# Performance work log

Hardware: AMD Instinct MI355X
Metric: run time of the kernel (lower is better)

## Reference

```python
import jax, jax.numpy as jnp
import numpy as np

D_MODEL = 1024
NHEAD = 16
HEAD_DIM = D_MODEL // NHEAD
SCALE = HEAD_DIM ** (-0.5)


def setup_inputs() -> dict:
    key = jax.random.key(0)
    k1, k2, k3 = jax.random.split(key, 3)
    B, T, C = 2, 2048, D_MODEL
    x = jax.random.normal(k1, (B, T, C), dtype=jnp.float32)
    W_qkv = jax.random.normal(k2, (3 * C, C), dtype=jnp.float32) * (C ** -0.5)
    b_qkv = jnp.zeros((3 * C,), dtype=jnp.float32)
    W_out = jax.random.normal(k3, (C, C), dtype=jnp.float32) * (C ** -0.5)
    b_out = jnp.zeros((C,), dtype=jnp.float32)
    return {"x": x, "W_qkv": W_qkv, "b_qkv": b_qkv, "W_out": W_out, "b_out": b_out}


def reference(x, W_qkv, b_qkv, W_out, b_out):
    B, T, C = x.shape
    H, hd = NHEAD, HEAD_DIM
    qkv = x @ W_qkv.T + b_qkv
    qkv = qkv.reshape(B, T, 3, H, hd).transpose(2, 0, 3, 1, 4)
    q, k, v = qkv[0], qkv[1], qkv[2]
    # scaled dot-product scores: (B,H,T,T)
    attn = jnp.einsum('bhqd,bhkd->bhqk', q, k) * SCALE
    # causal mask (is_causal=True): lower-triangular allowed
    causal = jnp.tril(jnp.ones((T, T), dtype=bool))
    attn = jnp.where(causal[None, None, :, :], attn, -jnp.inf)
    attn = jax.nn.softmax(attn, axis=-1)
    # (B,H,T,hd) -> (B,T,C)
    out = jnp.einsum('bhqk,bhkd->bhqd', attn, v)
    out = out.transpose(0, 2, 1, 3).reshape(B, T, C)
    out = out @ W_out.T + b_out
    return out
```

## Files before the change

### kernel.cpp

```cpp
#include <hip/hip_runtime.h>
#include <hip/hip_bf16.h>
#include <stdint.h>

#define D_MODEL 1024
#define NHEAD   16
#define HEAD_DIM 64
#define BATCH   2
#define SEQ     2048
#define M_TOK   (BATCH*SEQ)
#define N_QKV   (3*D_MODEL)
#define KDIM    1024
#define Q_SCALE (0.125f * 1.44269504088896f)

typedef __bf16 bf16_t;
typedef bf16_t bf16x8 __attribute__((ext_vector_type(8)));
typedef bf16_t bf16x4 __attribute__((ext_vector_type(4)));
typedef float  f32x4  __attribute__((ext_vector_type(4)));

__device__ __forceinline__ void gl_lds16(const void* g, void* l) {
    __builtin_amdgcn_global_load_lds(
        (__attribute__((address_space(1))) void*)(void*)(const_cast<void*>(g)),
        (__attribute__((address_space(3))) void*)l, 16, 0, 0);
}

#define N4_X  (M_TOK * KDIM / 4)
#define N4_W1 (N_QKV * KDIM / 4)
#define N4_W2 (D_MODEL * KDIM / 4)
__global__ void convert_all(const float* __restrict__ x,
                            const float* __restrict__ w1,
                            const float* __restrict__ w2,
                            bf16_t* __restrict__ ox,
                            bf16_t* __restrict__ o1,
                            bf16_t* __restrict__ o2) {
    int t = blockIdx.x * blockDim.x + threadIdx.x;
    const float* src;
    bf16_t* dst;
    int off;
    if (t < N4_X)                { src = x;  dst = ox; off = t; }
    else if (t < N4_X + N4_W1)   { src = w1; dst = o1; off = t - N4_X; }
    else                         { src = w2; dst = o2; off = t - N4_X - N4_W1; }
    float4 v = reinterpret_cast<const float4*>(src)[off];
    bf16x4 o = { (bf16_t)v.x, (bf16_t)v.y, (bf16_t)v.z, (bf16_t)v.w };
    reinterpret_cast<bf16x4*>(dst)[off] = o;
}

template <int MODE>
__global__ __launch_bounds__(256) void gemm_bt(
    const bf16_t* __restrict__ A,
    const bf16_t* __restrict__ Bw,
    const float*  __restrict__ bias,
    int N,
    bf16_t* __restrict__ qkv_out,
    bf16_t* __restrict__ vt_out,
    float*  __restrict__ f32_out)
{
    __shared__ bf16_t As[128 * 32];
    __shared__ bf16_t Bs[128 * 32];

    const int cpx = gridDim.x >> 3;
    const int bid = (blockIdx.x & 7) * cpx + (blockIdx.x >> 3);

    const int nbn = N / 128;
    const int bm = bid / nbn;
    const int bn = bid % nbn;
    const int m0 = bm * 128, n0 = bn * 128;
    const int tid = threadIdx.x, wave = tid >> 6, lane = tid & 63;
    const int wr = wave >> 1, wc = wave & 1;

    f32x4 acc[4][4] = {};

    const int srow = lane >> 2;
    const int scol = ((lane & 3) ^ ((lane >> 3) & 3)) * 8;
    const bf16_t* gA0 = A  + (size_t)(m0 + wave * 16 + srow) * KDIM + scol;
    const bf16_t* gB0 = Bw + (size_t)(n0 + wave * 16 + srow) * KDIM + scol;
    bf16_t* lA0 = &As[(wave * 16) * 32];
    bf16_t* lB0 = &Bs[(wave * 16) * 32];

    const int fr = lane & 15;
    const int ch = ((lane >> 4) ^ ((fr >> 1) & 3)) * 8;

    for (int k0 = 0; k0 < KDIM; k0 += 32) {
        gl_lds16(gA0 + k0,             lA0);
        gl_lds16(gA0 + 64 * KDIM + k0, lA0 + 64 * 32);
        gl_lds16(gB0 + k0,             lB0);
        gl_lds16(gB0 + 64 * KDIM + k0, lB0 + 64 * 32);
        __syncthreads();

        bf16x8 af[4], bfr[4];
#pragma unroll
        for (int i = 0; i < 4; i++)
            af[i] = *reinterpret_cast<const bf16x8*>(
                &As[(wr * 64 + i * 16 + fr) * 32 + ch]);
#pragma unroll
        for (int j = 0; j < 4; j++)
            bfr[j] = *reinterpret_cast<const bf16x8*>(
                &Bs[(wc * 64 + j * 16 + fr) * 32 + ch]);
#pragma unroll
        for (int i = 0; i < 4; i++)
#pragma unroll
            for (int j = 0; j < 4; j++)
                acc[i][j] = __builtin_amdgcn_mfma_f32_16x16x32_bf16(
                    af[i], bfr[j], acc[i][j], 0, 0, 0);
        __syncthreads();
    }

#pragma unroll
    for (int i = 0; i < 4; i++) {
#pragma unroll
        for (int j = 0; j < 4; j++) {
            const int col = n0 + wc * 64 + j * 16 + fr;
            const float bv = bias[col];
#pragma unroll
            for (int r = 0; r < 4; r++) {
                const int row = m0 + wr * 64 + i * 16 + (lane >> 4) * 4 + r;
                float v = acc[i][j][r] + bv;
                if (MODE == 0) {
                    const int s = col >> 10;
                    if (s == 0) {
                        qkv_out[(size_t)row * N_QKV + col] = (bf16_t)(v * Q_SCALE);
                    } else if (s == 1) {
                        qkv_out[(size_t)row * N_QKV + col] = (bf16_t)v;
                    } else {
                        const int rem = col & 1023;
                        const int h = rem >> 6, d = rem & 63;
                        const int b = row >> 11, t = row & 2047;
                        vt_out[((size_t)((b * NHEAD + h) * HEAD_DIM + d)) * SEQ + t] =
                            (bf16_t)v;
                    }
                } else {
                    f32_out[(size_t)row * N + col] = v;
                }
            }
        }
    }
}

__global__ __launch_bounds__(256) void attn_fwd(
    const bf16_t* __restrict__ qkv,
    const bf16_t* __restrict__ Vt,
    bf16_t* __restrict__ O)
{
    __shared__ bf16_t Ks[64 * 64];
    __shared__ bf16_t Vs[64 * 64];
    __shared__ bf16_t Ps[4][16 * 72];

    const int nqt = SEQ / 64;
    const int nbh = BATCH * NHEAD;
    const int qt = (nqt - 1) - (blockIdx.x / nbh);
    const int bh = blockIdx.x % nbh;
    const int b = bh >> 4, h = bh & 15;
    const int q0 = qt * 64;
    const int tid = threadIdx.x, wave = tid >> 6, lane = tid & 63;
    const int fr = lane & 15;
    const int kq = lane >> 4;
    const int sw = fr & 7;
    const int c0 = (kq ^ sw) * 8;
    const int c1 = ((kq + 4) ^ sw) * 8;

    bf16x8 qf[2];
    {
        const size_t qrow = (size_t)(b * SEQ + q0 + wave * 16 + fr);
        const int cbase = h * 64 + kq * 8;
        qf[0] = *reinterpret_cast<const bf16x8*>(&qkv[qrow * N_QKV + cbase]);
        qf[1] = *reinterpret_cast<const bf16x8*>(&qkv[qrow * N_QKV + cbase + 32]);
    }

    f32x4 acc_o[4] = {};
    float l_part = 0.f;

    const int srow = lane >> 3;
    const int scol = ((lane & 7) ^ srow) * 8;
    const bf16_t* gK = qkv + (size_t)(b * SEQ) * N_QKV + (D_MODEL + h * 64);
    const bf16_t* gV = Vt + (size_t)(bh * 64) * SEQ;

    const int ntiles = qt + 1;
    for (int it = 0; it < ntiles; ++it) {
        const int kv0 = it * 64;
#pragma unroll
        for (int c = 0; c < 2; c++) {
            const int row = c * 32 + wave * 8 + srow;
            gl_lds16(gK + (size_t)(kv0 + row) * N_QKV + scol,
                     &Ks[(c * 32 + wave * 8) * 64]);
            gl_lds16(gV + (size_t)row * SEQ + kv0 + scol,
                     &Vs[(c * 32 + wave * 8) * 64]);
        }
        __syncthreads();

        f32x4 s[4];
        __builtin_amdgcn_s_setprio(1);
#pragma unroll
        for (int j = 0; j < 4; j++) {
            bf16x8 k0f = *reinterpret_cast<const bf16x8*>(
                &Ks[(j * 16 + fr) * 64 + c0]);
            bf16x8 k1f = *reinterpret_cast<const bf16x8*>(
                &Ks[(j * 16 + fr) * 64 + c1]);
            f32x4 t = {0.f, 0.f, 0.f, 0.f};
            t = __builtin_amdgcn_mfma_f32_16x16x32_bf16(k0f, qf[0], t, 0, 0, 0);
            t = __builtin_amdgcn_mfma_f32_16x16x32_bf16(k1f, qf[1], t, 0, 0, 0);
            s[j] = t;
        }
        __builtin_amdgcn_s_setprio(0);

        if (it == ntiles - 1) {
            const int qg = wave * 16 + fr;
#pragma unroll
            for (int j = 0; j < 4; j++)
#pragma unroll
                for (int r = 0; r < 4; r++)
                    if (j * 16 + kq * 4 + r > qg) s[j][r] = -1e30f;
        }

        float rs = 0.f;
#pragma unroll
        for (int j = 0; j < 4; j++)
#pragma unroll
            for (int r = 0; r < 4; r++) {
                const float p = exp2f(s[j][r]);
                s[j][r] = p;
                rs += p;
            }
        l_part += rs;

#pragma unroll
        for (int j = 0; j < 4; j++) {
            bf16x4 pq = { (bf16_t)s[j][0], (bf16_t)s[j][1],
                          (bf16_t)s[j][2], (bf16_t)s[j][3] };
            *reinterpret_cast<bf16x4*>(&Ps[wave][fr * 72 + j * 16 + kq * 4]) = pq;
        }
        bf16x8 pb0 = *reinterpret_cast<const bf16x8*>(
            &Ps[wave][fr * 72 + kq * 8]);
        bf16x8 pb1 = *reinterpret_cast<const bf16x8*>(
            &Ps[wave][fr * 72 + 32 + kq * 8]);

        __builtin_amdgcn_s_setprio(1);
#pragma unroll
        for (int j = 0; j < 4; j++) {
            bf16x8 v0f = *reinterpret_cast<const bf16x8*>(
                &Vs[(j * 16 + fr) * 64 + c0]);
            bf16x8 v1f = *reinterpret_cast<const bf16x8*>(
                &Vs[(j * 16 + fr) * 64 + c1]);
            acc_o[j] = __builtin_amdgcn_mfma_f32_16x16x32_bf16(v0f, pb0, acc_o[j], 0, 0, 0);
            acc_o[j] = __builtin_amdgcn_mfma_f32_16x16x32_bf16(v1f, pb1, acc_o[j], 0, 0, 0);
        }
        __builtin_amdgcn_s_setprio(0);

        __syncthreads();
    }

    float l_run = l_part;
    l_run += __shfl_xor(l_run, 16);
    l_run += __shfl_xor(l_run, 32);
    const float inv = 1.0f / l_run;
    const size_t rowq = (size_t)(b * SEQ + q0 + wave * 16 + fr);
#pragma unroll
    for (int j = 0; j < 4; j++) {
        bf16x4 ov = { (bf16_t)(acc_o[j][0] * inv), (bf16_t)(acc_o[j][1] * inv),
                      (bf16_t)(acc_o[j][2] * inv), (bf16_t)(acc_o[j][3] * inv) };
        *reinterpret_cast<bf16x4*>(&O[rowq * D_MODEL + h * 64 + j * 16 + kq * 4]) = ov;
    }
}

extern "C" void kernel_launch(void* const* d_in, const int* in_sizes, int n_in,
                              void* d_out, int out_size, void* d_ws, size_t ws_size,
                              hipStream_t stream) {
    (void)in_sizes; (void)n_in; (void)out_size; (void)ws_size;
    const float* x    = (const float*)d_in[0];
    const float* Wqkv = (const float*)d_in[1];
    const float* bqkv = (const float*)d_in[2];
    const float* Wout = (const float*)d_in[3];
    const float* bout = (const float*)d_in[4];
    float* out = (float*)d_out;

    char* ws = (char*)d_ws;
    size_t off = 0;
    bf16_t* x_bf    = (bf16_t*)(ws + off); off += (size_t)M_TOK * KDIM * 2;
    bf16_t* wqkv_bf = (bf16_t*)(ws + off); off += (size_t)N_QKV * KDIM * 2;
    bf16_t* wout_bf = (bf16_t*)(ws + off); off += (size_t)D_MODEL * KDIM * 2;
    bf16_t* qkv     = (bf16_t*)(ws + off); off += (size_t)M_TOK * N_QKV * 2;
    bf16_t* vt      = (bf16_t*)(ws + off); off += (size_t)BATCH * NHEAD * HEAD_DIM * SEQ * 2;
    bf16_t* o_bf    = (bf16_t*)(ws + off); off += (size_t)M_TOK * D_MODEL * 2;

    convert_all<<<(N4_X + N4_W1 + N4_W2) / 256, 256, 0, stream>>>(
        x, Wqkv, Wout, x_bf, wqkv_bf, wout_bf);

    gemm_bt<0><<<(M_TOK / 128) * (N_QKV / 128), 256, 0, stream>>>(
        x_bf, wqkv_bf, bqkv, N_QKV, qkv, vt, nullptr);

    attn_fwd<<<BATCH * NHEAD * (SEQ / 64), 256, 0, stream>>>(qkv, vt, o_bf);

    gemm_bt<1><<<(M_TOK / 128) * (D_MODEL / 128), 256, 0, stream>>>(
        o_bf, wout_bf, bout, D_MODEL, nullptr, nullptr, out);
}
```

Baseline: 118.2 us.

## Process 32 query rows per wave in attention to reuse K/V fragments

```diff
diff --git a/kernel.cpp b/kernel.cpp
--- a/kernel.cpp
+++ b/kernel.cpp
@@ -135,14 +135,14 @@
     }
 }
 
-__global__ __launch_bounds__(256) void attn_fwd(
+__global__ __launch_bounds__(128) void attn_fwd(
     const bf16_t* __restrict__ qkv,
     const bf16_t* __restrict__ Vt,
     bf16_t* __restrict__ O)
 {
     __shared__ bf16_t Ks[64 * 64];
     __shared__ bf16_t Vs[64 * 64];
-    __shared__ bf16_t Ps[4][16 * 72];
+    __shared__ bf16_t Ps[2][32 * 72];
 
     const int nqt = SEQ / 64;
     const int nbh = BATCH * NHEAD;
@@ -157,16 +157,19 @@
     const int c0 = (kq ^ sw) * 8;
     const int c1 = ((kq + 4) ^ sw) * 8;
 
-    bf16x8 qf[2];
+    bf16x8 qf0[2], qf1[2];
     {
-        const size_t qrow = (size_t)(b * SEQ + q0 + wave * 16 + fr);
         const int cbase = h * 64 + kq * 8;
-        qf[0] = *reinterpret_cast<const bf16x8*>(&qkv[qrow * N_QKV + cbase]);
-        qf[1] = *reinterpret_cast<const bf16x8*>(&qkv[qrow * N_QKV + cbase + 32]);
-    }
-
-    f32x4 acc_o[4] = {};
-    float l_part = 0.f;
+        const size_t r0 = (size_t)(b * SEQ + q0 + wave * 32 + fr);
+        const size_t r1 = r0 + 16;
+        qf0[0] = *reinterpret_cast<const bf16x8*>(&qkv[r0 * N_QKV + cbase]);
+        qf0[1] = *reinterpret_cast<const bf16x8*>(&qkv[r0 * N_QKV + cbase + 32]);
+        qf1[0] = *reinterpret_cast<const bf16x8*>(&qkv[r1 * N_QKV + cbase]);
+        qf1[1] = *reinterpret_cast<const bf16x8*>(&qkv[r1 * N_QKV + cbase + 32]);
+    }
+
+    f32x4 acc0[4] = {}, acc1[4] = {};
+    float l0 = 0.f, l1 = 0.f;
 
     const int srow = lane >> 3;
     const int scol = ((lane & 7) ^ srow) * 8;
@@ -177,60 +180,84 @@
     for (int it = 0; it < ntiles; ++it) {
         const int kv0 = it * 64;
 #pragma unroll
-        for (int c = 0; c < 2; c++) {
-            const int row = c * 32 + wave * 8 + srow;
+        for (int c = 0; c < 4; c++) {
+            const int row = wave * 32 + c * 8 + srow;
             gl_lds16(gK + (size_t)(kv0 + row) * N_QKV + scol,
-                     &Ks[(c * 32 + wave * 8) * 64]);
+                     &Ks[(wave * 32 + c * 8) * 64]);
             gl_lds16(gV + (size_t)row * SEQ + kv0 + scol,
-                     &Vs[(c * 32 + wave * 8) * 64]);
+                     &Vs[(wave * 32 + c * 8) * 64]);
         }
         __syncthreads();
 
-        f32x4 s[4];
+        bf16x8 kf0[4], kf1[4];
+#pragma unroll
+        for (int j = 0; j < 4; j++) {
+            kf0[j] = *reinterpret_cast<const bf16x8*>(
+                &Ks[(j * 16 + fr) * 64 + c0]);
+            kf1[j] = *reinterpret_cast<const bf16x8*>(
+                &Ks[(j * 16 + fr) * 64 + c1]);
+        }
+
+        f32x4 s0[4], s1[4];
         __builtin_amdgcn_s_setprio(1);
 #pragma unroll
         for (int j = 0; j < 4; j++) {
-            bf16x8 k0f = *reinterpret_cast<const bf16x8*>(
-                &Ks[(j * 16 + fr) * 64 + c0]);
-            bf16x8 k1f = *reinterpret_cast<const bf16x8*>(
-                &Ks[(j * 16 + fr) * 64 + c1]);
             f32x4 t = {0.f, 0.f, 0.f, 0.f};
-            t = __builtin_amdgcn_mfma_f32_16x16x32_bf16(k0f, qf[0], t, 0, 0, 0);
-            t = __builtin_amdgcn_mfma_f32_16x16x32_bf16(k1f, qf[1], t, 0, 0, 0);
-            s[j] = t;
+            t = __builtin_amdgcn_mfma_f32_16x16x32_bf16(kf0[j], qf0[0], t, 0, 0, 0);
+            t = __builtin_amdgcn_mfma_f32_16x16x32_bf16(kf1[j], qf0[1], t, 0, 0, 0);
+            s0[j] = t;
+            f32x4 u = {0.f, 0.f, 0.f, 0.f};
+            u = __builtin_amdgcn_mfma_f32_16x16x32_bf16(kf0[j], qf1[0], u, 0, 0, 0);
+            u = __builtin_amdgcn_mfma_f32_16x16x32_bf16(kf1[j], qf1[1], u, 0, 0, 0);
+            s1[j] = u;
         }
         __builtin_amdgcn_s_setprio(0);
 
         if (it == ntiles - 1) {
-            const int qg = wave * 16 + fr;
+            const int qg0 = wave * 32 + fr;
+            const int qg1 = qg0 + 16;
 #pragma unroll
             for (int j = 0; j < 4; j++)
 #pragma unroll
-                for (int r = 0; r < 4; r++)
-                    if (j * 16 + kq * 4 + r > qg) s[j][r] = -1e30f;
-        }
-
-        float rs = 0.f;
+                for (int r = 0; r < 4; r++) {
+                    const int kvl = j * 16 + kq * 4 + r;
+                    if (kvl > qg0) s0[j][r] = -1e30f;
+                    if (kvl > qg1) s1[j][r] = -1e30f;
+                }
+        }
+
+        float rs0 = 0.f, rs1 = 0.f;
 #pragma unroll
         for (int j = 0; j < 4; j++)
 #pragma unroll
             for (int r = 0; r < 4; r++) {
-                const float p = exp2f(s[j][r]);
-                s[j][r] = p;
-                rs += p;
+                const float p0 = exp2f(s0[j][r]);
+                const float p1 = exp2f(s1[j][r]);
+                s0[j][r] = p0;
+                s1[j][r] = p1;
+                rs0 += p0;
+                rs1 += p1;
             }
-        l_part += rs;
-
-#pragma unroll
-        for (int j = 0; j < 4; j++) {
-            bf16x4 pq = { (bf16_t)s[j][0], (bf16_t)s[j][1],
-                          (bf16_t)s[j][2], (bf16_t)s[j][3] };
-            *reinterpret_cast<bf16x4*>(&Ps[wave][fr * 72 + j * 16 + kq * 4]) = pq;
-        }
+        l0 += rs0;
+        l1 += rs1;
+
+#pragma unroll
+        for (int j = 0; j < 4; j++) {
+            bf16x4 p0 = { (bf16_t)s0[j][0], (bf16_t)s0[j][1],
+                          (bf16_t)s0[j][2], (bf16_t)s0[j][3] };
+            *reinterpret_cast<bf16x4*>(&Ps[wave][fr * 72 + j * 16 + kq * 4]) = p0;
+            bf16x4 p1 = { (bf16_t)s1[j][0], (bf16_t)s1[j][1],
+                          (bf16_t)s1[j][2], (bf16_t)s1[j][3] };
+            *reinterpret_cast<bf16x4*>(&Ps[wave][(16 + fr) * 72 + j * 16 + kq * 4]) = p1;
+        }
+        bf16x8 pa0 = *reinterpret_cast<const bf16x8*>(
+            &Ps[wave][fr * 72 + kq * 8]);
+        bf16x8 pa1 = *reinterpret_cast<const bf16x8*>(
+            &Ps[wave][fr * 72 + 32 + kq * 8]);
         bf16x8 pb0 = *reinterpret_cast<const bf16x8*>(
-            &Ps[wave][fr * 72 + kq * 8]);
+            &Ps[wave][(16 + fr) * 72 + kq * 8]);
         bf16x8 pb1 = *reinterpret_cast<const bf16x8*>(
-            &Ps[wave][fr * 72 + 32 + kq * 8]);
+            &Ps[wave][(16 + fr) * 72 + 32 + kq * 8]);
 
         __builtin_amdgcn_s_setprio(1);
 #pragma unroll
@@ -239,24 +266,32 @@
                 &Vs[(j * 16 + fr) * 64 + c0]);
             bf16x8 v1f = *reinterpret_cast<const bf16x8*>(
                 &Vs[(j * 16 + fr) * 64 + c1]);
-            acc_o[j] = __builtin_amdgcn_mfma_f32_16x16x32_bf16(v0f, pb0, acc_o[j], 0, 0, 0);
-            acc_o[j] = __builtin_amdgcn_mfma_f32_16x16x32_bf16(v1f, pb1, acc_o[j], 0, 0, 0);
+            acc0[j] = __builtin_amdgcn_mfma_f32_16x16x32_bf16(v0f, pa0, acc0[j], 0, 0, 0);
+            acc0[j] = __builtin_amdgcn_mfma_f32_16x16x32_bf16(v1f, pa1, acc0[j], 0, 0, 0);
+            acc1[j] = __builtin_amdgcn_mfma_f32_16x16x32_bf16(v0f, pb0, acc1[j], 0, 0, 0);
+            acc1[j] = __builtin_amdgcn_mfma_f32_16x16x32_bf16(v1f, pb1, acc1[j], 0, 0, 0);
         }
         __builtin_amdgcn_s_setprio(0);
 
         __syncthreads();
     }
 
-    float l_run = l_part;
-    l_run += __shfl_xor(l_run, 16);
-    l_run += __shfl_xor(l_run, 32);
-    const float inv = 1.0f / l_run;
-    const size_t rowq = (size_t)(b * SEQ + q0 + wave * 16 + fr);
+    l0 += __shfl_xor(l0, 16);
+    l0 += __shfl_xor(l0, 32);
+    l1 += __shfl_xor(l1, 16);
+    l1 += __shfl_xor(l1, 32);
+    const float inv0 = 1.0f / l0;
+    const float inv1 = 1.0f / l1;
+    const size_t row0 = (size_t)(b * SEQ + q0 + wave * 32 + fr);
+    const size_t row1 = row0 + 16;
 #pragma unroll
     for (int j = 0; j < 4; j++) {
-        bf16x4 ov = { (bf16_t)(acc_o[j][0] * inv), (bf16_t)(acc_o[j][1] * inv),
-                      (bf16_t)(acc_o[j][2] * inv), (bf16_t)(acc_o[j][3] * inv) };
-        *reinterpret_cast<bf16x4*>(&O[rowq * D_MODEL + h * 64 + j * 16 + kq * 4]) = ov;
+        bf16x4 o0 = { (bf16_t)(acc0[j][0] * inv0), (bf16_t)(acc0[j][1] * inv0),
+                      (bf16_t)(acc0[j][2] * inv0), (bf16_t)(acc0[j][3] * inv0) };
+        *reinterpret_cast<bf16x4*>(&O[row0 * D_MODEL + h * 64 + j * 16 + kq * 4]) = o0;
+        bf16x4 o1 = { (bf16_t)(acc1[j][0] * inv1), (bf16_t)(acc1[j][1] * inv1),
+                      (bf16_t)(acc1[j][2] * inv1), (bf16_t)(acc1[j][3] * inv1) };
+        *reinterpret_cast<bf16x4*>(&O[row1 * D_MODEL + h * 64 + j * 16 + kq * 4]) = o1;
     }
 }
 
@@ -286,7 +321,7 @@
     gemm_bt<0><<<(M_TOK / 128) * (N_QKV / 128), 256, 0, stream>>>(
         x_bf, wqkv_bf, bqkv, N_QKV, qkv, vt, nullptr);
 
-    attn_fwd<<<BATCH * NHEAD * (SEQ / 64), 256, 0, stream>>>(qkv, vt, o_bf);
+    attn_fwd<<<BATCH * NHEAD * (SEQ / 64), 128, 0, stream>>>(qkv, vt, o_bf);
 
     gemm_bt<1><<<(M_TOK / 128) * (D_MODEL / 128), 256, 0, stream>>>(
         o_bf, wout_bf, bout, D_MODEL, nullptr, nullptr, out);
```

New measurement: 133.4 us. 12.9% more time.

## Split KV range across two wave groups per attention block and merge partials

Applied to the files above, without the earlier changes.

```diff
diff --git a/kernel.cpp b/kernel.cpp
--- a/kernel.cpp
+++ b/kernel.cpp
@@ -135,14 +135,14 @@
     }
 }
 
-__global__ __launch_bounds__(256) void attn_fwd(
+__global__ __launch_bounds__(512) void attn_fwd(
     const bf16_t* __restrict__ qkv,
     const bf16_t* __restrict__ Vt,
     bf16_t* __restrict__ O)
 {
-    __shared__ bf16_t Ks[64 * 64];
-    __shared__ bf16_t Vs[64 * 64];
-    __shared__ bf16_t Ps[4][16 * 72];
+    __shared__ bf16_t Ks[2][64 * 64];
+    __shared__ bf16_t Vs[2][64 * 64];
+    __shared__ bf16_t Ps[8][16 * 72];
 
     const int nqt = SEQ / 64;
     const int nbh = BATCH * NHEAD;
@@ -151,6 +151,8 @@
     const int b = bh >> 4, h = bh & 15;
     const int q0 = qt * 64;
     const int tid = threadIdx.x, wave = tid >> 6, lane = tid & 63;
+    const int group = wave >> 2;
+    const int w4 = wave & 3;
     const int fr = lane & 15;
     const int kq = lane >> 4;
     const int sw = fr & 7;
@@ -159,7 +161,7 @@
 
     bf16x8 qf[2];
     {
-        const size_t qrow = (size_t)(b * SEQ + q0 + wave * 16 + fr);
+        const size_t qrow = (size_t)(b * SEQ + q0 + w4 * 16 + fr);
         const int cbase = h * 64 + kq * 8;
         qf[0] = *reinterpret_cast<const bf16x8*>(&qkv[qrow * N_QKV + cbase]);
         qf[1] = *reinterpret_cast<const bf16x8*>(&qkv[qrow * N_QKV + cbase + 32]);
@@ -173,90 +175,118 @@
     const bf16_t* gK = qkv + (size_t)(b * SEQ) * N_QKV + (D_MODEL + h * 64);
     const bf16_t* gV = Vt + (size_t)(bh * 64) * SEQ;
 
-    const int ntiles = qt + 1;
-    for (int it = 0; it < ntiles; ++it) {
-        const int kv0 = it * 64;
-#pragma unroll
-        for (int c = 0; c < 2; c++) {
-            const int row = c * 32 + wave * 8 + srow;
-            gl_lds16(gK + (size_t)(kv0 + row) * N_QKV + scol,
-                     &Ks[(c * 32 + wave * 8) * 64]);
-            gl_lds16(gV + (size_t)row * SEQ + kv0 + scol,
-                     &Vs[(c * 32 + wave * 8) * 64]);
+    const int nh0 = (qt + 2) >> 1;
+    const int my_n = (group == 0) ? nh0 : (qt + 1 - nh0);
+    const int base_t = (group == 0) ? 0 : nh0;
+
+    for (int it = 0; it < nh0; ++it) {
+        const bool act = (it < my_n);
+        const int g_it = base_t + it;
+        const int kv0 = g_it * 64;
+        if (act) {
+#pragma unroll
+            for (int c = 0; c < 2; c++) {
+                const int row = c * 32 + w4 * 8 + srow;
+                gl_lds16(gK + (size_t)(kv0 + row) * N_QKV + scol,
+                         &Ks[group][(c * 32 + w4 * 8) * 64]);
+                gl_lds16(gV + (size_t)row * SEQ + kv0 + scol,
+                         &Vs[group][(c * 32 + w4 * 8) * 64]);
+            }
         }
         __syncthreads();
 
-        f32x4 s[4];
-        __builtin_amdgcn_s_setprio(1);
+        if (act) {
+            f32x4 s[4];
+            __builtin_amdgcn_s_setprio(1);
+#pragma unroll
+            for (int j = 0; j < 4; j++) {
+                bf16x8 k0f = *reinterpret_cast<const bf16x8*>(
+                    &Ks[group][(j * 16 + fr) * 64 + c0]);
+                bf16x8 k1f = *reinterpret_cast<const bf16x8*>(
+                    &Ks[group][(j * 16 + fr) * 64 + c1]);
+                f32x4 t = {0.f, 0.f, 0.f, 0.f};
+                t = __builtin_amdgcn_mfma_f32_16x16x32_bf16(k0f, qf[0], t, 0, 0, 0);
+                t = __builtin_amdgcn_mfma_f32_16x16x32_bf16(k1f, qf[1], t, 0, 0, 0);
+                s[j] = t;
+            }
+            __builtin_amdgcn_s_setprio(0);
+
+            if (g_it == qt) {
+                const int qg = w4 * 16 + fr;
+#pragma unroll
+                for (int j = 0; j < 4; j++)
+#pragma unroll
+                    for (int r = 0; r < 4; r++)
+                        if (j * 16 + kq * 4 + r > qg) s[j][r] = -1e30f;
+            }
+
+            float rs = 0.f;
+#pragma unroll
+            for (int j = 0; j < 4; j++)
+#pragma unroll
+                for (int r = 0; r < 4; r++) {
+                    const float p = exp2f(s[j][r]);
+                    s[j][r] = p;
+                    rs += p;
+                }
+            l_part += rs;
+
+#pragma unroll
+            for (int j = 0; j < 4; j++) {
+                bf16x4 pq = { (bf16_t)s[j][0], (bf16_t)s[j][1],
+                              (bf16_t)s[j][2], (bf16_t)s[j][3] };
+                *reinterpret_cast<bf16x4*>(&Ps[wave][fr * 72 + j * 16 + kq * 4]) = pq;
+            }
+            bf16x8 pb0 = *reinterpret_cast<const bf16x8*>(
+                &Ps[wave][fr * 72 + kq * 8]);
+            bf16x8 pb1 = *reinterpret_cast<const bf16x8*>(
+                &Ps[wave][fr * 72 + 32 + kq * 8]);
+
+            __builtin_amdgcn_s_setprio(1);
+#pragma unroll
+            for (int j = 0; j < 4; j++) {
+                bf16x8 v0f = *reinterpret_cast<const bf16x8*>(
+                    &Vs[group][(j * 16 + fr) * 64 + c0]);
+                bf16x8 v1f = *reinterpret_cast<const bf16x8*>(
+                    &Vs[group][(j * 16 + fr) * 64 + c1]);
+                acc_o[j] = __builtin_amdgcn_mfma_f32_16x16x32_bf16(v0f, pb0, acc_o[j], 0, 0, 0);
+                acc_o[j] = __builtin_amdgcn_mfma_f32_16x16x32_bf16(v1f, pb1, acc_o[j], 0, 0, 0);
+            }
+            __builtin_amdgcn_s_setprio(0);
+        }
+
+        __syncthreads();
+    }
+
+    float* Cf = reinterpret_cast<float*>(&Ps[0][0]);
+    const int pbase = w4 * 1088;
+    if (group == 1) {
+#pragma unroll
+        for (int j = 0; j < 4; j++)
+#pragma unroll
+            for (int r = 0; r < 4; r++)
+                Cf[pbase + (j * 4 + r) * 64 + lane] = acc_o[j][r];
+        Cf[pbase + 1024 + lane] = l_part;
+    }
+    __syncthreads();
+    if (group == 0) {
+#pragma unroll
+        for (int j = 0; j < 4; j++)
+#pragma unroll
+            for (int r = 0; r < 4; r++)
+                acc_o[j][r] += Cf[pbase + (j * 4 + r) * 64 + lane];
+        l_part += Cf[pbase + 1024 + lane];
+
+        l_part += __shfl_xor(l_part, 16);
+        l_part += __shfl_xor(l_part, 32);
+        const float inv = 1.0f / l_part;
+        const size_t rowq = (size_t)(b * SEQ + q0 + w4 * 16 + fr);
 #pragma unroll
         for (int j = 0; j < 4; j++) {
-            bf16x8 k0f = *reinterpret_cast<const bf16x8*>(
-                &Ks[(j * 16 + fr) * 64 + c0]);
-            bf16x8 k1f = *reinterpret_cast<const bf16x8*>(
-                &Ks[(j * 16 + fr) * 64 + c1]);
-            f32x4 t = {0.f, 0.f, 0.f, 0.f};
-            t = __builtin_amdgcn_mfma_f32_16x16x32_bf16(k0f, qf[0], t, 0, 0, 0);
-            t = __builtin_amdgcn_mfma_f32_16x16x32_bf16(k1f, qf[1], t, 0, 0, 0);
-            s[j] = t;
+            bf16x4 ov = { (bf16_t)(acc_o[j][0] * inv), (bf16_t)(acc_o[j][1] * inv),
+                          (bf16_t)(acc_o[j][2] * inv), (bf16_t)(acc_o[j][3] * inv) };
+            *reinterpret_cast<bf16x4*>(&O[rowq * D_MODEL + h * 64 + j * 16 + kq * 4]) = ov;
         }
-        __builtin_amdgcn_s_setprio(0);
-
-        if (it == ntiles - 1) {
-            const int qg = wave * 16 + fr;
-#pragma unroll
-            for (int j = 0; j < 4; j++)
-#pragma unroll
-                for (int r = 0; r < 4; r++)
-                    if (j * 16 + kq * 4 + r > qg) s[j][r] = -1e30f;
-        }
-
-        float rs = 0.f;
-#pragma unroll
-        for (int j = 0; j < 4; j++)
-#pragma unroll
-            for (int r = 0; r < 4; r++) {
-                const float p = exp2f(s[j][r]);
-                s[j][r] = p;
-                rs += p;
-            }
-        l_part += rs;
-
-#pragma unroll
-        for (int j = 0; j < 4; j++) {
-            bf16x4 pq = { (bf16_t)s[j][0], (bf16_t)s[j][1],
-                          (bf16_t)s[j][2], (bf16_t)s[j][3] };
-            *reinterpret_cast<bf16x4*>(&Ps[wave][fr * 72 + j * 16 + kq * 4]) = pq;
-        }
-        bf16x8 pb0 = *reinterpret_cast<const bf16x8*>(
-            &Ps[wave][fr * 72 + kq * 8]);
-        bf16x8 pb1 = *reinterpret_cast<const bf16x8*>(
-            &Ps[wave][fr * 72 + 32 + kq * 8]);
-
-        __builtin_amdgcn_s_setprio(1);
-#pragma unroll
-        for (int j = 0; j < 4; j++) {
-            bf16x8 v0f = *reinterpret_cast<const bf16x8*>(
-                &Vs[(j * 16 + fr) * 64 + c0]);
-            bf16x8 v1f = *reinterpret_cast<const bf16x8*>(
-                &Vs[(j * 16 + fr) * 64 + c1]);
-            acc_o[j] = __builtin_amdgcn_mfma_f32_16x16x32_bf16(v0f, pb0, acc_o[j], 0, 0, 0);
-            acc_o[j] = __builtin_amdgcn_mfma_f32_16x16x32_bf16(v1f, pb1, acc_o[j], 0, 0, 0);
-        }
-        __builtin_amdgcn_s_setprio(0);
-
-        __syncthreads();
-    }
-
-    float l_run = l_part;
-    l_run += __shfl_xor(l_run, 16);
-    l_run += __shfl_xor(l_run, 32);
-    const float inv = 1.0f / l_run;
-    const size_t rowq = (size_t)(b * SEQ + q0 + wave * 16 + fr);
-#pragma unroll
-    for (int j = 0; j < 4; j++) {
-        bf16x4 ov = { (bf16_t)(acc_o[j][0] * inv), (bf16_t)(acc_o[j][1] * inv),
-                      (bf16_t)(acc_o[j][2] * inv), (bf16_t)(acc_o[j][3] * inv) };
-        *reinterpret_cast<bf16x4*>(&O[rowq * D_MODEL + h * 64 + j * 16 + kq * 4]) = ov;
     }
 }
 
@@ -286,7 +316,7 @@
     gemm_bt<0><<<(M_TOK / 128) * (N_QKV / 128), 256, 0, stream>>>(
         x_bf, wqkv_bf, bqkv, N_QKV, qkv, vt, nullptr);
 
-    attn_fwd<<<BATCH * NHEAD * (SEQ / 64), 256, 0, stream>>>(qkv, vt, o_bf);
+    attn_fwd<<<BATCH * NHEAD * (SEQ / 64), 512, 0, stream>>>(qkv, vt, o_bf);
 
     gemm_bt<1><<<(M_TOK / 128) * (D_MODEL / 128), 256, 0, stream>>>(
         o_bf, wout_bf, bout, D_MODEL, nullptr, nullptr, out);
```

Measured after the change: 113.9 us. 3.7% less time.
